# Kernel optimization log

Measured on AMD Instinct MI355X. Metric: run time of the kernel, lower is better.

## Reference

```python
import jax, jax.numpy as jnp
import numpy as np
import math

D_MODEL = 1024
N_HEADS = 16
D_K = D_MODEL // N_HEADS


def setup_inputs() -> dict:
    key = jax.random.key(0)
    ks = jax.random.split(key, 12)
    B, S, D = 2, 2048, D_MODEL
    inp = {
        'q': jax.random.normal(ks[0], (B, S, D), jnp.float32),
        'k': jax.random.normal(ks[1], (B, S, D), jnp.float32),
        'v': jax.random.normal(ks[2], (B, S, D), jnp.float32),
        'mask': jnp.ones((B, 1, 1, S), jnp.int32),
    }
    sc = 1.0 / math.sqrt(D)
    inp['wq_w'] = jax.random.normal(ks[3], (D, D), jnp.float32) * sc
    inp['wq_b'] = jnp.zeros((D,), jnp.float32)
    inp['wk_w'] = jax.random.normal(ks[4], (D, D), jnp.float32) * sc
    inp['wk_b'] = jnp.zeros((D,), jnp.float32)
    inp['wv_w'] = jax.random.normal(ks[5], (D, D), jnp.float32) * sc
    inp['wv_b'] = jnp.zeros((D,), jnp.float32)
    inp['wo_w'] = jax.random.normal(ks[6], (D, D), jnp.float32) * sc
    inp['wo_b'] = jnp.zeros((D,), jnp.float32)
    return inp


def reference(q, k, v, mask, wq_w, wq_b, wk_w, wk_b, wv_w, wv_b, wo_w, wo_b):
    B, S, D = q.shape
    H, Dk = N_HEADS, D_K
    scale = math.sqrt(Dk)
    # projections; weights stored as (out, in) like torch Linear -> x @ W^T + b
    def proj(x, w, b):
        y = jnp.einsum('bsd,ed->bse', x, w) + b
        return y.reshape(B, S, H, Dk).transpose(0, 2, 1, 3)  # (B,H,S,Dk)
    qh = proj(q, wq_w, wq_b)
    kh = proj(k, wk_w, wk_b)
    vh = proj(v, wv_w, wv_b)
    scores = jnp.einsum('bhqd,bhkd->bhqk', qh, kh) / scale  # (B,H,S,S)
    scores = jnp.where(mask == 0, jnp.float32(-1e9), scores)
    attention = jax.nn.softmax(scores, axis=-1)
    # dropout is identity at inference (eval mode)
    out = jnp.einsum('bhqk,bhkd->bhqd', attention, vh)  # (B,H,S,Dk)
    out = out.transpose(0, 2, 1, 3).reshape(B, S, D)
    out = jnp.einsum('bsd,ed->bse', out, wo_w) + wo_b
    return out, attention
```

## Files before the change

### kernel.cpp

```cpp
#include <hip/hip_runtime.h>
#include <stdint.h>

#define SB 2048
#define DM 1024
#define NHH 16
#define DKK 64

typedef unsigned short u16;
using short8  = __attribute__((ext_vector_type(8))) short;
using short4v = __attribute__((ext_vector_type(4))) short;
using f32x4   = __attribute__((ext_vector_type(4))) float;

__device__ __forceinline__ u16 f2bf(float f) {
    union { float f; unsigned u; } v; v.f = f;
    unsigned u = v.u;
    return (u16)((u + 0x7FFFu + ((u >> 16) & 1u)) >> 16);
}

__device__ __forceinline__ void stage16(const float* __restrict__ src, u16* dst) {
    const float4* s4 = (const float4*)src;
#pragma unroll
    for (int t = 0; t < 2; ++t) {
        const float4 a = s4[2 * t], b = s4[2 * t + 1];
        short8 p;
        p[0] = (short)f2bf(a.x); p[1] = (short)f2bf(a.y);
        p[2] = (short)f2bf(a.z); p[3] = (short)f2bf(a.w);
        p[4] = (short)f2bf(b.x); p[5] = (short)f2bf(b.y);
        p[6] = (short)f2bf(b.z); p[7] = (short)f2bf(b.w);
        *(short8*)(dst + 8 * t) = p;
    }
}

__global__ __launch_bounds__(256) void proj_kernel(
    const float* __restrict__ X, const float* __restrict__ W,
    const float* __restrict__ Bv, u16* __restrict__ Y, int vmode)
{
    __shared__ __align__(16) u16 As[64 * 72];
    __shared__ __align__(16) u16 Bs[64 * 72];

    const int tid  = threadIdx.x;
    const int lane = tid & 63, wv = tid >> 6;
    const int li = lane & 15, g = lane >> 4;
    const int wr = wv >> 1, wc = wv & 1;
    const int m0 = blockIdx.y * 64, n0 = blockIdx.x * 64;

    f32x4 acc[2][2] = {};

    const int rs = tid >> 2;
    const int cs = (tid & 3) * 16;

    for (int k0 = 0; k0 < DM; k0 += 64) {
        stage16(&X[(m0 + rs) * DM + k0 + cs], &As[rs * 72 + cs]);
        stage16(&W[(n0 + rs) * DM + k0 + cs], &Bs[rs * 72 + cs]);
        __syncthreads();
#pragma unroll
        for (int kk = 0; kk < 2; ++kk) {
            short8 a0 = *(const short8*)&As[(wr * 32 + li) * 72 + kk * 32 + g * 8];
            short8 a1 = *(const short8*)&As[(wr * 32 + 16 + li) * 72 + kk * 32 + g * 8];
            short8 b0 = *(const short8*)&Bs[(wc * 32 + li) * 72 + kk * 32 + g * 8];
            short8 b1 = *(const short8*)&Bs[(wc * 32 + 16 + li) * 72 + kk * 32 + g * 8];
            acc[0][0] = __builtin_amdgcn_mfma_f32_16x16x32_bf16(a0, b0, acc[0][0], 0, 0, 0);
            acc[0][1] = __builtin_amdgcn_mfma_f32_16x16x32_bf16(a0, b1, acc[0][1], 0, 0, 0);
            acc[1][0] = __builtin_amdgcn_mfma_f32_16x16x32_bf16(a1, b0, acc[1][0], 0, 0, 0);
            acc[1][1] = __builtin_amdgcn_mfma_f32_16x16x32_bf16(a1, b1, acc[1][1], 0, 0, 0);
        }
        __syncthreads();
    }

#pragma unroll
    for (int i = 0; i < 2; ++i)
#pragma unroll
        for (int j = 0; j < 2; ++j) {
            const int n = n0 + wc * 32 + j * 16 + li;
            const float bv = Bv[n];
            const int mbase = m0 + wr * 32 + i * 16 + g * 4;
            const int h = n >> 6, dk = n & 63;
            if (vmode == 0) {
#pragma unroll
                for (int r = 0; r < 4; ++r) {
                    const int m = mbase + r;
                    const int b = m >> 11, s = m & 2047;
                    Y[(((b * NHH + h) * SB) + s) * DKK + dk] = f2bf(acc[i][j][r] + bv);
                }
            } else {
                const int b = mbase >> 11, s = mbase & 2047;
                short4v pk;
                pk.x = (short)f2bf(acc[i][j][0] + bv);
                pk.y = (short)f2bf(acc[i][j][1] + bv);
                pk.z = (short)f2bf(acc[i][j][2] + bv);
                pk.w = (short)f2bf(acc[i][j][3] + bv);
                *(short4v*)&Y[(((b * NHH + h) * DKK) + dk) * SB + s] = pk;
            }
        }
}

__global__ __launch_bounds__(256) void attn_kernel(
    const u16* __restrict__ qh, const u16* __restrict__ kh,
    const int* __restrict__ mask, float* __restrict__ attn_out)
{
    __shared__ __align__(16) float sm[4][32];
    __shared__ __align__(16) float sl[4][32];

    const int tid = threadIdx.x, lane = tid & 63, w = tid >> 6;
    const int li = lane & 15, g = lane >> 4;
    const int bh = blockIdx.y;
    const int q0 = blockIdx.x * 32;
    const int b  = bh >> 4;
    const float sc2 = 0.125f * 1.44269504088896f;
    const float NEGI = -1.0e30f;

    short8 qa[2][2];
#pragma unroll
    for (int qs = 0; qs < 2; ++qs)
#pragma unroll
        for (int kk = 0; kk < 2; ++kk)
            qa[qs][kk] = *(const short8*)&qh[((bh * SB) + q0 + qs * 16 + li) * DKK + kk * 32 + g * 8];

    float mloc[2][4], lloc[2][4];
#pragma unroll
    for (int qs = 0; qs < 2; ++qs)
#pragma unroll
        for (int r = 0; r < 4; ++r) { mloc[qs][r] = NEGI; lloc[qs][r] = 0.f; }

    const int kbase = w * 512;

    for (int kt = 0; kt < 32; ++kt) {
        const int key0 = kbase + kt * 16;
        const short8 kb0 = *(const short8*)&kh[((bh * SB) + key0 + li) * DKK + g * 8];
        const short8 kb1 = *(const short8*)&kh[((bh * SB) + key0 + li) * DKK + 32 + g * 8];
        const int mv = mask[b * SB + key0 + li];
#pragma unroll
        for (int qs = 0; qs < 2; ++qs) {
            f32x4 acc = {};
            acc = __builtin_amdgcn_mfma_f32_16x16x32_bf16(qa[qs][0], kb0, acc, 0, 0, 0);
            acc = __builtin_amdgcn_mfma_f32_16x16x32_bf16(qa[qs][1], kb1, acc, 0, 0, 0);
#pragma unroll
            for (int r = 0; r < 4; ++r) {
                const float s2 = (mv == 0) ? -1.442695e9f : acc[r] * sc2;
                const float mo = mloc[qs][r];
                const float mn = fmaxf(mo, s2);
                lloc[qs][r] = lloc[qs][r] * exp2f(mo - mn) + exp2f(s2 - mn);
                mloc[qs][r] = mn;
            }
        }
    }
#pragma unroll
    for (int qs = 0; qs < 2; ++qs)
#pragma unroll
        for (int r = 0; r < 4; ++r) {
            float m = mloc[qs][r], l = lloc[qs][r];
#pragma unroll
            for (int xm = 1; xm < 16; xm <<= 1) {
                const float om = __shfl_xor(m, xm);
                const float ol = __shfl_xor(l, xm);
                const float mn = fmaxf(m, om);
                l = l * exp2f(m - mn) + ol * exp2f(om - mn);
                m = mn;
            }
            mloc[qs][r] = m; lloc[qs][r] = l;
        }
    if (li == 0) {
#pragma unroll
        for (int qs = 0; qs < 2; ++qs)
#pragma unroll
            for (int r = 0; r < 4; ++r) {
                sm[w][qs * 16 + g * 4 + r] = mloc[qs][r];
                sl[w][qs * 16 + g * 4 + r] = lloc[qs][r];
            }
    }
    __syncthreads();

    float M2[2][4], Li[2][4];
#pragma unroll
    for (int qs = 0; qs < 2; ++qs)
#pragma unroll
        for (int r = 0; r < 4; ++r) {
            const int rr = qs * 16 + g * 4 + r;
            const float M = fmaxf(fmaxf(sm[0][rr], sm[1][rr]), fmaxf(sm[2][rr], sm[3][rr]));
            const float L = sl[0][rr] * exp2f(sm[0][rr] - M) + sl[1][rr] * exp2f(sm[1][rr] - M)
                          + sl[2][rr] * exp2f(sm[2][rr] - M) + sl[3][rr] * exp2f(sm[3][rr] - M);
            M2[qs][r] = M;
            Li[qs][r] = 1.0f / L;
        }

    for (int kt = 0; kt < 32; ++kt) {
        const int key0 = kbase + kt * 16;
        const short8 kb0 = *(const short8*)&kh[((bh * SB) + key0 + li) * DKK + g * 8];
        const short8 kb1 = *(const short8*)&kh[((bh * SB) + key0 + li) * DKK + 32 + g * 8];
        const int mv = mask[b * SB + key0 + li];
#pragma unroll
        for (int qs = 0; qs < 2; ++qs) {
            f32x4 acc = {};
            acc = __builtin_amdgcn_mfma_f32_16x16x32_bf16(qa[qs][0], kb0, acc, 0, 0, 0);
            acc = __builtin_amdgcn_mfma_f32_16x16x32_bf16(qa[qs][1], kb1, acc, 0, 0, 0);
#pragma unroll
            for (int r = 0; r < 4; ++r) {
                const float s2 = (mv == 0) ? -1.442695e9f : acc[r] * sc2;
                const float p = exp2f(s2 - M2[qs][r]) * Li[qs][r];
                const int qrow = q0 + qs * 16 + g * 4 + r;
                attn_out[((size_t)(bh * SB + qrow)) * SB + key0 + li] = p;
            }
        }
    }
}

__global__ __launch_bounds__(256) void pv_kernel(
    const float* __restrict__ Pmat, const u16* __restrict__ vt, u16* __restrict__ oh)
{
    __shared__ __align__(16) u16 As[64 * 72];
    __shared__ __align__(16) u16 Bs[64 * 72];

    const int tid  = threadIdx.x;
    const int lane = tid & 63, wv = tid >> 6;
    const int li = lane & 15, g = lane >> 4;
    const int wr = wv >> 1, wc = wv & 1;
    const int bh = blockIdx.y;
    const int m0 = blockIdx.x * 64;
    const size_t pbase = (size_t)bh * SB * SB;

    f32x4 acc[2][2] = {};
    const int rs = tid >> 2;
    const int cs = (tid & 3) * 16;
    const int r0 = tid >> 3;
    const int c0 = (tid & 7) * 8;

    for (int k0 = 0; k0 < SB; k0 += 64) {
        stage16(&Pmat[pbase + (size_t)(m0 + rs) * SB + k0 + cs], &As[rs * 72 + cs]);
        *(short8*)&Bs[r0 * 72 + c0]        = *(const short8*)&vt[(bh * DKK + r0) * SB + k0 + c0];
        *(short8*)&Bs[(r0 + 32) * 72 + c0] = *(const short8*)&vt[(bh * DKK + r0 + 32) * SB + k0 + c0];
        __syncthreads();
#pragma unroll
        for (int kk = 0; kk < 2; ++kk) {
            short8 a0 = *(const short8*)&As[(wr * 32 + li) * 72 + kk * 32 + g * 8];
            short8 a1 = *(const short8*)&As[(wr * 32 + 16 + li) * 72 + kk * 32 + g * 8];
            short8 b0 = *(const short8*)&Bs[(wc * 32 + li) * 72 + kk * 32 + g * 8];
            short8 b1 = *(const short8*)&Bs[(wc * 32 + 16 + li) * 72 + kk * 32 + g * 8];
            acc[0][0] = __builtin_amdgcn_mfma_f32_16x16x32_bf16(a0, b0, acc[0][0], 0, 0, 0);
            acc[0][1] = __builtin_amdgcn_mfma_f32_16x16x32_bf16(a0, b1, acc[0][1], 0, 0, 0);
            acc[1][0] = __builtin_amdgcn_mfma_f32_16x16x32_bf16(a1, b0, acc[1][0], 0, 0, 0);
            acc[1][1] = __builtin_amdgcn_mfma_f32_16x16x32_bf16(a1, b1, acc[1][1], 0, 0, 0);
        }
        __syncthreads();
    }

#pragma unroll
    for (int i = 0; i < 2; ++i)
#pragma unroll
        for (int j = 0; j < 2; ++j) {
            const int n = wc * 32 + j * 16 + li;
            const int mbase = m0 + wr * 32 + i * 16 + g * 4;
#pragma unroll
            for (int r = 0; r < 4; ++r)
                oh[((bh * SB) + mbase + r) * DKK + n] = f2bf(acc[i][j][r]);
        }
}

__global__ __launch_bounds__(256) void oproj_kernel(
    const u16* __restrict__ OH, const float* __restrict__ W,
    const float* __restrict__ Bv, float* __restrict__ Y)
{
    __shared__ __align__(16) u16 As[64 * 72];
    __shared__ __align__(16) u16 Bs[64 * 72];

    const int tid  = threadIdx.x;
    const int lane = tid & 63, wv = tid >> 6;
    const int li = lane & 15, g = lane >> 4;
    const int wr = wv >> 1, wc = wv & 1;
    const int m0 = blockIdx.y * 64, n0 = blockIdx.x * 64;

    f32x4 acc[2][2] = {};
    const int rs = tid >> 2;
    const int cs = (tid & 3) * 16;
    const int r0 = tid >> 3;
    const int c0 = (tid & 7) * 8;

    for (int k0 = 0; k0 < DM; k0 += 64) {
        const int h = k0 >> 6;
        {
            const int m = m0 + r0, bb = m >> 11, s = m & 2047;
            *(short8*)&As[r0 * 72 + c0] =
                *(const short8*)&OH[(((bb * NHH + h) * SB) + s) * DKK + c0];
        }
        {
            const int m = m0 + r0 + 32, bb = m >> 11, s = m & 2047;
            *(short8*)&As[(r0 + 32) * 72 + c0] =
                *(const short8*)&OH[(((bb * NHH + h) * SB) + s) * DKK + c0];
        }
        stage16(&W[(n0 + rs) * DM + k0 + cs], &Bs[rs * 72 + cs]);
        __syncthreads();
#pragma unroll
        for (int kk = 0; kk < 2; ++kk) {
            short8 a0 = *(const short8*)&As[(wr * 32 + li) * 72 + kk * 32 + g * 8];
            short8 a1 = *(const short8*)&As[(wr * 32 + 16 + li) * 72 + kk * 32 + g * 8];
            short8 b0 = *(const short8*)&Bs[(wc * 32 + li) * 72 + kk * 32 + g * 8];
            short8 b1 = *(const short8*)&Bs[(wc * 32 + 16 + li) * 72 + kk * 32 + g * 8];
            acc[0][0] = __builtin_amdgcn_mfma_f32_16x16x32_bf16(a0, b0, acc[0][0], 0, 0, 0);
            acc[0][1] = __builtin_amdgcn_mfma_f32_16x16x32_bf16(a0, b1, acc[0][1], 0, 0, 0);
            acc[1][0] = __builtin_amdgcn_mfma_f32_16x16x32_bf16(a1, b0, acc[1][0], 0, 0, 0);
            acc[1][1] = __builtin_amdgcn_mfma_f32_16x16x32_bf16(a1, b1, acc[1][1], 0, 0, 0);
        }
        __syncthreads();
    }

#pragma unroll
    for (int i = 0; i < 2; ++i)
#pragma unroll
        for (int j = 0; j < 2; ++j) {
            const int n = n0 + wc * 32 + j * 16 + li;
            const float bv = Bv[n];
            const int mbase = m0 + wr * 32 + i * 16 + g * 4;
#pragma unroll
            for (int r = 0; r < 4; ++r)
                Y[(mbase + r) * DM + n] = acc[i][j][r] + bv;
        }
}

extern "C" void kernel_launch(void* const* d_in, const int* in_sizes, int n_in,
                              void* d_out, int out_size, void* d_ws, size_t ws_size,
                              hipStream_t stream) {
    const float* q    = (const float*)d_in[0];
    const float* k    = (const float*)d_in[1];
    const float* v    = (const float*)d_in[2];
    const int*   mask = (const int*)d_in[3];
    const float* wq   = (const float*)d_in[4];
    const float* bq   = (const float*)d_in[5];
    const float* wk   = (const float*)d_in[6];
    const float* bk   = (const float*)d_in[7];
    const float* wv   = (const float*)d_in[8];
    const float* bv   = (const float*)d_in[9];
    const float* wo   = (const float*)d_in[10];
    const float* bo   = (const float*)d_in[11];

    float* out  = (float*)d_out;
    float* attn = out + 4194304;

    u16* ws = (u16*)d_ws;
    u16* qh = ws;
    u16* kh = ws + 1 * 4194304;
    u16* vt = ws + 2 * 4194304;
    u16* oh = ws;

    dim3 blk(256);
    proj_kernel<<<dim3(16, 64), blk, 0, stream>>>(q, wq, bq, qh, 0);
    proj_kernel<<<dim3(16, 64), blk, 0, stream>>>(k, wk, bk, kh, 0);
    proj_kernel<<<dim3(16, 64), blk, 0, stream>>>(v, wv, bv, vt, 1);
    attn_kernel<<<dim3(64, 32), blk, 0, stream>>>(qh, kh, mask, attn);
    pv_kernel<<<dim3(32, 32), blk, 0, stream>>>(attn, vt, oh);
    oproj_kernel<<<dim3(16, 64), blk, 0, stream>>>(oh, wo, bo, out);
}
```

Measured before the change: 1.046 ms.

## Fuse PV into attention kernel and batch QKV projections into one launch

The P·V product now runs inside the attention kernel. Each wave keeps its probability tile in bf16 in shared memory and accumulates its key-slice contribution to the output with MFMA. The four waves' partial outputs are then reduced through shared memory and written as bf16. This removes the separate pv_kernel, which re-read the full fp32 attention matrix from global memory. The three projection launches are also merged into one grid with a z dimension selecting q, k or v. The cost is more registers and shared memory per block in the attention kernel, plus a serialized cross-wave reduction.

```diff
diff --git a/kernel.cpp b/kernel.cpp
--- a/kernel.cpp
+++ b/kernel.cpp
@@ -31,17 +31,27 @@
     }
 }
 
-__global__ __launch_bounds__(256) void proj_kernel(
-    const float* __restrict__ X, const float* __restrict__ W,
-    const float* __restrict__ Bv, u16* __restrict__ Y, int vmode)
+__global__ __launch_bounds__(256) void proj3_kernel(
+    const float* __restrict__ q, const float* __restrict__ k, const float* __restrict__ v,
+    const float* __restrict__ wq, const float* __restrict__ bq,
+    const float* __restrict__ wk, const float* __restrict__ bk,
+    const float* __restrict__ wv, const float* __restrict__ bv,
+    u16* __restrict__ qh, u16* __restrict__ kh, u16* __restrict__ vt)
 {
     __shared__ __align__(16) u16 As[64 * 72];
     __shared__ __align__(16) u16 Bs[64 * 72];
 
+    const int z = blockIdx.z;
+    const float* X  = (z == 0) ? q  : (z == 1) ? k  : v;
+    const float* W  = (z == 0) ? wq : (z == 1) ? wk : wv;
+    const float* Bv = (z == 0) ? bq : (z == 1) ? bk : bv;
+    u16*         Y  = (z == 0) ? qh : (z == 1) ? kh : vt;
+    const int vmode = (z == 2);
+
     const int tid  = threadIdx.x;
-    const int lane = tid & 63, wv = tid >> 6;
+    const int lane = tid & 63, wv_ = tid >> 6;
     const int li = lane & 15, g = lane >> 4;
-    const int wr = wv >> 1, wc = wv & 1;
+    const int wr = wv_ >> 1, wc = wv_ & 1;
     const int m0 = blockIdx.y * 64, n0 = blockIdx.x * 64;
 
     f32x4 acc[2][2] = {};
@@ -72,7 +82,7 @@
 #pragma unroll
         for (int j = 0; j < 2; ++j) {
             const int n = n0 + wc * 32 + j * 16 + li;
-            const float bv = Bv[n];
+            const float bvv = Bv[n];
             const int mbase = m0 + wr * 32 + i * 16 + g * 4;
             const int h = n >> 6, dk = n & 63;
             if (vmode == 0) {
@@ -80,26 +90,29 @@
                 for (int r = 0; r < 4; ++r) {
                     const int m = mbase + r;
                     const int b = m >> 11, s = m & 2047;
-                    Y[(((b * NHH + h) * SB) + s) * DKK + dk] = f2bf(acc[i][j][r] + bv);
+                    Y[(((b * NHH + h) * SB) + s) * DKK + dk] = f2bf(acc[i][j][r] + bvv);
                 }
             } else {
                 const int b = mbase >> 11, s = mbase & 2047;
                 short4v pk;
-                pk.x = (short)f2bf(acc[i][j][0] + bv);
-                pk.y = (short)f2bf(acc[i][j][1] + bv);
-                pk.z = (short)f2bf(acc[i][j][2] + bv);
-                pk.w = (short)f2bf(acc[i][j][3] + bv);
+                pk.x = (short)f2bf(acc[i][j][0] + bvv);
+                pk.y = (short)f2bf(acc[i][j][1] + bvv);
+                pk.z = (short)f2bf(acc[i][j][2] + bvv);
+                pk.w = (short)f2bf(acc[i][j][3] + bvv);
                 *(short4v*)&Y[(((b * NHH + h) * DKK) + dk) * SB + s] = pk;
             }
         }
 }
 
-__global__ __launch_bounds__(256) void attn_kernel(
+__global__ __launch_bounds__(256) void attn_pv_kernel(
     const u16* __restrict__ qh, const u16* __restrict__ kh,
-    const int* __restrict__ mask, float* __restrict__ attn_out)
+    const u16* __restrict__ vt, const int* __restrict__ mask,
+    float* __restrict__ attn_out, u16* __restrict__ oh)
 {
-    __shared__ __align__(16) float sm[4][32];
-    __shared__ __align__(16) float sl[4][32];
+    __shared__ __align__(16) u16 Ps[4][32 * 40];
+    __shared__ float sm[4][32];
+    __shared__ float sl[4][32];
+    __shared__ __align__(16) float comb[32 * 68];
 
     const int tid = threadIdx.x, lane = tid & 63, w = tid >> 6;
     const int li = lane & 15, g = lane >> 4;
@@ -183,76 +196,70 @@
             Li[qs][r] = 1.0f / L;
         }
 
-    for (int kt = 0; kt < 32; ++kt) {
-        const int key0 = kbase + kt * 16;
-        const short8 kb0 = *(const short8*)&kh[((bh * SB) + key0 + li) * DKK + g * 8];
-        const short8 kb1 = *(const short8*)&kh[((bh * SB) + key0 + li) * DKK + 32 + g * 8];
-        const int mv = mask[b * SB + key0 + li];
+    f32x4 oacc[2][4] = {};
+
+    for (int pt = 0; pt < 16; ++pt) {
+        const int pk0 = kbase + pt * 32;
+
+        short8 vb[4];
+#pragma unroll
+        for (int jt = 0; jt < 4; ++jt)
+            vb[jt] = *(const short8*)&vt[((bh * DKK) + jt * 16 + li) * SB + pk0 + g * 8];
+
+#pragma unroll
+        for (int kk2 = 0; kk2 < 2; ++kk2) {
+            const int key0 = pk0 + kk2 * 16;
+            const short8 kb0 = *(const short8*)&kh[((bh * SB) + key0 + li) * DKK + g * 8];
+            const short8 kb1 = *(const short8*)&kh[((bh * SB) + key0 + li) * DKK + 32 + g * 8];
+            const int mv = mask[b * SB + key0 + li];
+#pragma unroll
+            for (int qs = 0; qs < 2; ++qs) {
+                f32x4 acc = {};
+                acc = __builtin_amdgcn_mfma_f32_16x16x32_bf16(qa[qs][0], kb0, acc, 0, 0, 0);
+                acc = __builtin_amdgcn_mfma_f32_16x16x32_bf16(qa[qs][1], kb1, acc, 0, 0, 0);
+#pragma unroll
+                for (int r = 0; r < 4; ++r) {
+                    const float s2 = (mv == 0) ? -1.442695e9f : acc[r] * sc2;
+                    const float p = exp2f(s2 - M2[qs][r]) * Li[qs][r];
+                    const int row = qs * 16 + g * 4 + r;
+                    attn_out[((size_t)(bh * SB + q0 + row)) * SB + key0 + li] = p;
+                    Ps[w][row * 40 + kk2 * 16 + li] = f2bf(p);
+                }
+            }
+        }
+
 #pragma unroll
         for (int qs = 0; qs < 2; ++qs) {
-            f32x4 acc = {};
-            acc = __builtin_amdgcn_mfma_f32_16x16x32_bf16(qa[qs][0], kb0, acc, 0, 0, 0);
-            acc = __builtin_amdgcn_mfma_f32_16x16x32_bf16(qa[qs][1], kb1, acc, 0, 0, 0);
-#pragma unroll
-            for (int r = 0; r < 4; ++r) {
-                const float s2 = (mv == 0) ? -1.442695e9f : acc[r] * sc2;
-                const float p = exp2f(s2 - M2[qs][r]) * Li[qs][r];
-                const int qrow = q0 + qs * 16 + g * 4 + r;
-                attn_out[((size_t)(bh * SB + qrow)) * SB + key0 + li] = p;
-            }
-        }
-    }
-}
-
-__global__ __launch_bounds__(256) void pv_kernel(
-    const float* __restrict__ Pmat, const u16* __restrict__ vt, u16* __restrict__ oh)
-{
-    __shared__ __align__(16) u16 As[64 * 72];
-    __shared__ __align__(16) u16 Bs[64 * 72];
-
-    const int tid  = threadIdx.x;
-    const int lane = tid & 63, wv = tid >> 6;
-    const int li = lane & 15, g = lane >> 4;
-    const int wr = wv >> 1, wc = wv & 1;
-    const int bh = blockIdx.y;
-    const int m0 = blockIdx.x * 64;
-    const size_t pbase = (size_t)bh * SB * SB;
-
-    f32x4 acc[2][2] = {};
-    const int rs = tid >> 2;
-    const int cs = (tid & 3) * 16;
-    const int r0 = tid >> 3;
-    const int c0 = (tid & 7) * 8;
-
-    for (int k0 = 0; k0 < SB; k0 += 64) {
-        stage16(&Pmat[pbase + (size_t)(m0 + rs) * SB + k0 + cs], &As[rs * 72 + cs]);
-        *(short8*)&Bs[r0 * 72 + c0]        = *(const short8*)&vt[(bh * DKK + r0) * SB + k0 + c0];
-        *(short8*)&Bs[(r0 + 32) * 72 + c0] = *(const short8*)&vt[(bh * DKK + r0 + 32) * SB + k0 + c0];
-        __syncthreads();
-#pragma unroll
-        for (int kk = 0; kk < 2; ++kk) {
-            short8 a0 = *(const short8*)&As[(wr * 32 + li) * 72 + kk * 32 + g * 8];
-            short8 a1 = *(const short8*)&As[(wr * 32 + 16 + li) * 72 + kk * 32 + g * 8];
-            short8 b0 = *(const short8*)&Bs[(wc * 32 + li) * 72 + kk * 32 + g * 8];
-            short8 b1 = *(const short8*)&Bs[(wc * 32 + 16 + li) * 72 + kk * 32 + g * 8];
-            acc[0][0] = __builtin_amdgcn_mfma_f32_16x16x32_bf16(a0, b0, acc[0][0], 0, 0, 0);
-            acc[0][1] = __builtin_amdgcn_mfma_f32_16x16x32_bf16(a0, b1, acc[0][1], 0, 0, 0);
-            acc[1][0] = __builtin_amdgcn_mfma_f32_16x16x32_bf16(a1, b0, acc[1][0], 0, 0, 0);
-            acc[1][1] = __builtin_amdgcn_mfma_f32_16x16x32_bf16(a1, b1, acc[1][1], 0, 0, 0);
-        }
-        __syncthreads();
-    }
-
-#pragma unroll
-    for (int i = 0; i < 2; ++i)
-#pragma unroll
-        for (int j = 0; j < 2; ++j) {
-            const int n = wc * 32 + j * 16 + li;
-            const int mbase = m0 + wr * 32 + i * 16 + g * 4;
-#pragma unroll
-            for (int r = 0; r < 4; ++r)
-                oh[((bh * SB) + mbase + r) * DKK + n] = f2bf(acc[i][j][r]);
-        }
+            const short8 pa = *(const short8*)&Ps[w][(qs * 16 + li) * 40 + g * 8];
+#pragma unroll
+            for (int jt = 0; jt < 4; ++jt)
+                oacc[qs][jt] = __builtin_amdgcn_mfma_f32_16x16x32_bf16(pa, vb[jt], oacc[qs][jt], 0, 0, 0);
+        }
+    }
+
+    for (int wt = 0; wt < 4; ++wt) {
+        if (w == wt) {
+#pragma unroll
+            for (int qs = 0; qs < 2; ++qs)
+#pragma unroll
+                for (int jt = 0; jt < 4; ++jt)
+#pragma unroll
+                    for (int r = 0; r < 4; ++r) {
+                        const int idx = (qs * 16 + g * 4 + r) * 68 + jt * 16 + li;
+                        if (wt == 0) comb[idx] = oacc[qs][jt][r];
+                        else         comb[idx] += oacc[qs][jt][r];
+                    }
+        }
+        __syncthreads();
+    }
+
+    {
+        const int row = tid >> 3, c0 = (tid & 7) * 8;
+        short8 pk;
+#pragma unroll
+        for (int j = 0; j < 8; ++j) pk[j] = (short)f2bf(comb[row * 68 + c0 + j]);
+        *(short8*)&oh[((bh * SB) + q0 + row) * DKK + c0] = pk;
+    }
 }
 
 __global__ __launch_bounds__(256) void oproj_kernel(
@@ -341,10 +348,7 @@
     u16* oh = ws;
 
     dim3 blk(256);
-    proj_kernel<<<dim3(16, 64), blk, 0, stream>>>(q, wq, bq, qh, 0);
-    proj_kernel<<<dim3(16, 64), blk, 0, stream>>>(k, wk, bk, kh, 0);
-    proj_kernel<<<dim3(16, 64), blk, 0, stream>>>(v, wv, bv, vt, 1);
-    attn_kernel<<<dim3(64, 32), blk, 0, stream>>>(qh, kh, mask, attn);
-    pv_kernel<<<dim3(32, 32), blk, 0, stream>>>(attn, vt, oh);
+    proj3_kernel<<<dim3(16, 64, 3), blk, 0, stream>>>(q, k, v, wq, bq, wk, bk, wv, bv, qh, kh, vt);
+    attn_pv_kernel<<<dim3(64, 32), blk, 0, stream>>>(qh, kh, vt, mask, attn, oh);
     oproj_kernel<<<dim3(16, 64), blk, 0, stream>>>(oh, wo, bo, out);
 }
```

Measured after the change: 958.8 us. 8.3% less time.
